# Kernel tuning notes

Hardware: AMD Instinct MI355X
Metric: run time of the kernel (lower is better)

The kernel has to match this reference:

```python
import jax, jax.numpy as jnp
import numpy as np

B, T, DIM, DZ = 512, 256, 128, 256
H = 2 * DZ  # LSTM hidden size (per direction)
RESIDUAL = False


def _lstm_cell(xt, h, c, Wih, Whh, bih, bhh):
    # PyTorch gate order: input, forget, cell, output
    g = xt @ Wih.T + bih + h @ Whh.T + bhh
    i, f, gg, o = jnp.split(g, 4, axis=-1)
    c2 = jax.nn.sigmoid(f) * c + jax.nn.sigmoid(i) * jnp.tanh(gg)
    h2 = jax.nn.sigmoid(o) * jnp.tanh(c2)
    return h2, c2


def _masked_lstm(xs, lengths, Wih, Whh, bih, bhh):
    # Packed-sequence semantics: state frozen and output zero past each length.
    Bn, Tn, _ = xs.shape
    Hn = Whh.shape[1]

    def step(carry, inp):
        h, c = carry
        xt, t = inp
        h2, c2 = _lstm_cell(xt, h, c, Wih, Whh, bih, bhh)
        m = (t < lengths)[:, None]
        h = jnp.where(m, h2, h)
        c = jnp.where(m, c2, c)
        return (h, c), jnp.where(m, h2, 0.0)

    init = (jnp.zeros((Bn, Hn), xs.dtype), jnp.zeros((Bn, Hn), xs.dtype))
    _, hs = jax.lax.scan(step, init, (xs.swapaxes(0, 1), jnp.arange(Tn)))
    return hs.swapaxes(0, 1)  # [B,T,H]


def setup_inputs() -> dict:
    key = jax.random.key(0)
    ks = jax.random.split(key, 24)
    rn = lambda k, *s: jax.random.normal(k, s, jnp.float32) * 0.02
    z = jnp.zeros
    return {
        "x": jax.random.normal(ks[0], (B, T, DIM), jnp.float32),
        "x_lengths": jax.random.randint(ks[1], (B,), 1, T + 1),
        "norm_g": jnp.ones((T, DIM)), "norm_b": z((T, DIM)),
        "We": rn(ks[2], DZ, DIM), "be": z((DZ,)),
        "Wih_f": rn(ks[3], 4 * H, DZ), "Whh_f": rn(ks[4], 4 * H, H),
        "bih_f": z((4 * H,)), "bhh_f": z((4 * H,)),
        "Wih_b": rn(ks[5], 4 * H, DZ), "Whh_b": rn(ks[6], 4 * H, H),
        "bih_b": z((4 * H,)), "bhh_b": z((4 * H,)),
        "W1e": rn(ks[7], H, 2 * H), "b1e": z((H,)),
        "W2e": rn(ks[8], DZ, H), "b2e": z((DZ,)),
        "Wd": rn(ks[9], DZ, DZ), "bd": z((DZ,)),
        "Wp1": rn(ks[10], DZ, DZ), "bp1": z((DZ,)),
        "Wp2": rn(ks[11], DIM, DZ), "bp2": z((DIM,)),
        "Wih_d": rn(ks[12], 4 * H, DZ + DIM), "Whh_d": rn(ks[13], 4 * H, H),
        "bih_d": z((4 * H,)), "bhh_d": z((4 * H,)),
        "W1d": rn(ks[14], DZ, H), "b1d": z((DZ,)),
        "W2d": rn(ks[15], DIM, DZ), "b2d": z((DIM,)),
    }


def _forward(x, x_lengths, norm_g, norm_b, We, be,
             Wih_f, Whh_f, bih_f, bhh_f, Wih_b, Whh_b, bih_b, bhh_b,
             W1e, b1e, W2e, b2e,
             Wd, bd, Wp1, bp1, Wp2, bp2,
             Wih_d, Whh_d, bih_d, bhh_d, W1d, b1d, W2d, b2d):
    # ----- encoder -----
    # LayerNorm over the last two dims [T, DIM] per sample
    mu = x.mean(axis=(1, 2), keepdims=True)
    var = x.var(axis=(1, 2), keepdims=True)
    xn = (x - mu) / jnp.sqrt(var + 1e-5) * norm_g + norm_b
    xe = jax.nn.relu(xn @ We.T + be)  # [B,T,DZ]

    hs_f = _masked_lstm(xe, x_lengths, Wih_f, Whh_f, bih_f, bhh_f)
    # backward direction: reverse each valid prefix, run, scatter back
    rev_idx = jnp.clip(x_lengths[:, None] - 1 - jnp.arange(T)[None, :], 0)  # [B,T]
    xe_rev = jnp.take_along_axis(xe, rev_idx[:, :, None], axis=1)
    hs_b_rev = _masked_lstm(xe_rev, x_lengths, Wih_b, Whh_b, bih_b, bhh_b)
    hs_b = jnp.take_along_axis(hs_b_rev, rev_idx[:, :, None], axis=1)
    valid = (jnp.arange(T)[None, :] < x_lengths[:, None])[:, :, None]
    out = jnp.concatenate([hs_f, jnp.where(valid, hs_b, 0.0)], axis=-1)  # [B,T,2H]
    out = out.sum(axis=1) / x_lengths[:, None].astype(x.dtype)
    out = jax.nn.relu(out @ W1e.T + b1e)
    zlat = out @ W2e.T + b2e  # [B,DZ]

    x0 = jax.nn.relu(zlat @ Wd.T + bd)
    pose0 = jax.nn.relu(x0 @ Wp1.T + bp1) @ Wp2.T + bp2  # [B,DIM]
    h0 = jnp.zeros((x.shape[0], H), x.dtype)

    def dstep(carry, _):
        h, c, pose = carry
        inp = jnp.concatenate([x0, pose], axis=1)
        h2, c2 = _lstm_cell(inp, h, c, Wih_d, Whh_d, bih_d, bhh_d)
        h_ = jax.nn.relu(h2 @ W1d.T + b1d)
        new_pose = h_ @ W2d.T + b2d
        if RESIDUAL:
            new_pose = new_pose + pose
        return (h2, c2, new_pose), new_pose

    _, poses = jax.lax.scan(dstep, (h0, h0, pose0), None, length=T)
    return poses.swapaxes(0, 1)  # [B,T,DIM]


def reference(x, x_lengths, norm_g, norm_b, We, be,
              Wih_f, Whh_f, bih_f, bhh_f, Wih_b, Whh_b, bih_b, bhh_b,
              W1e, b1e, W2e, b2e,
              Wd, bd, Wp1, bp1, Wp2, bp2,
              Wih_d, Whh_d, bih_d, bhh_d, W1d, b1d, W2d, b2d):
    dec = _forward(x, x_lengths, norm_g, norm_b, We, be,
                   Wih_f, Whh_f, bih_f, bhh_f, Wih_b, Whh_b, bih_b, bhh_b,
                   W1e, b1e, W2e, b2e,
                   Wd, bd, Wp1, bp1, Wp2, bp2,
                   Wih_d, Whh_d, bih_d, bhh_d, W1d, b1d, W2d, b2d)
    return (x, dec, x_lengths)
```

## Files before the change

### kernel.cpp

```cpp
#include <hip/hip_runtime.h>
#include <stdint.h>
#include <math.h>

typedef unsigned short u16;
typedef unsigned long long u64;
typedef short s16x8 __attribute__((ext_vector_type(8)));
typedef __bf16 bv8 __attribute__((ext_vector_type(8)));
typedef float f32x4 __attribute__((ext_vector_type(4)));

#define DEV static __device__ __forceinline__

DEV float b2f(u16 x){ union{unsigned u; float f;} v; v.u=((unsigned)x)<<16; return v.f; }
DEV u16 f2b(float f){ union{float f; unsigned u;} v; v.f=f; unsigned u=v.u; u += 0x7fff + ((u>>16)&1u); return (u16)(u>>16); }
DEV float sigm(float x){ return 1.f/(1.f+__expf(-x)); }
DEV float tanh_(float x){ float cx=fminf(fmaxf(x,-20.f),20.f); float e=__expf(2.f*cx); return (e-1.f)/(e+1.f); }
DEV f32x4 mfma16(bv8 a, bv8 b, f32x4 c){ return __builtin_amdgcn_mfma_f32_16x16x32_bf16(a,b,c,0,0,0); }
DEV bv8 ldf(const u16* p){ return __builtin_bit_cast(bv8, *(const s16x8*)p); }
DEV bv8 cvt(const s16x8& v){ return __builtin_bit_cast(bv8, v); }

DEV unsigned ald4(const unsigned* p){ return __hip_atomic_load(p, __ATOMIC_RELAXED, __HIP_MEMORY_SCOPE_AGENT); }

DEV void gld16(s16x8& d, const u16* p){
  asm volatile("global_load_dwordx4 %0, %1, off sc0 sc1" : "=&v"(d) : "v"(p));
}
DEV void gst8(u16* p, u64 v){
  asm volatile("global_store_dwordx2 %0, %1, off sc0 sc1" :: "v"(p), "v"(v) : "memory");
}
template<int N> DEV void wvm(){
  asm volatile("s_waitcnt vmcnt(%0)" :: "i"(N) : "memory");
  __builtin_amdgcn_sched_barrier(0);
}

DEV void arrive(unsigned* flags, int my, unsigned e){
  asm volatile("s_waitcnt vmcnt(0)" ::: "memory");
  __syncthreads();
  if (threadIdx.x==0)
    __hip_atomic_store(&flags[my*32], e, __ATOMIC_RELAXED, __HIP_MEMORY_SCOPE_AGENT);
}
DEV void waitflags(unsigned* flags, int lo, int n, unsigned e){
  int t = (int)threadIdx.x;
  if (t>=lo && t<lo+n){
    while (ald4(&flags[t*32]) < e) __builtin_amdgcn_s_sleep(1);
  }
  __syncthreads();
}

struct CvtJobs { const float* s[14]; u16* d[14]; int start[14]; };

__global__ __launch_bounds__(256) void cvt_w(CvtJobs J){
  int blk = blockIdx.x, tid = threadIdx.x;
  int j = 0;
  #pragma unroll
  for (int k=1;k<14;k++) if (blk >= J.start[k]) j = k;
  size_t idx = (size_t)(blk - J.start[j])*2048 + (size_t)tid*8;
  const f32x4* ps = (const f32x4*)(J.s[j] + idx);
  f32x4 a = ps[0], b = ps[1];
  s16x8 o;
  #pragma unroll
  for (int i=0;i<4;i++){ o[i]=(short)f2b(a[i]); o[4+i]=(short)f2b(b[i]); }
  *(s16x8*)(J.d[j] + idx) = o;
}

__global__ __launch_bounds__(256) void tr_w2d(const u16* __restrict__ in, u16* __restrict__ out){
  int idx = blockIdx.x*256 + threadIdx.x;
  int r = idx>>7, p = idx&127;
  out[idx] = in[p*256 + r];
}

__global__ __launch_bounds__(256) void pb_k(const float* __restrict__ Wihd, const float* __restrict__ b2d,
                                            float* __restrict__ pb){
  int g = blockIdx.x*256 + threadIdx.x;
  const float* row = Wihd + (size_t)g*384 + 256;
  float s = 0.f;
  for (int p=0;p<128;p++) s += row[p]*b2d[p];
  pb[g] = s;
}

__global__ __launch_bounds__(256) void ln_stats(const float* __restrict__ x,
                                                float* __restrict__ mu, float* __restrict__ rstd){
  int b = blockIdx.x;
  const float* xb = x + (size_t)b*32768;
  float s1=0.f, s2=0.f;
  for (int i = threadIdx.x*4; i < 32768; i += 256*4){
    f32x4 v = *(const f32x4*)(xb+i);
    #pragma unroll
    for (int j=0;j<4;j++){ float f = v[j]; s1+=f; s2+=f*f; }
  }
  #pragma unroll
  for (int o=32;o>0;o>>=1){ s1 += __shfl_down(s1,o); s2 += __shfl_down(s2,o); }
  __shared__ float r1[4], r2[4];
  int w = threadIdx.x>>6;
  if ((threadIdx.x&63)==0){ r1[w]=s1; r2[w]=s2; }
  __syncthreads();
  if (threadIdx.x==0){
    float a=0.f,c=0.f;
    for (int i=0;i<4;i++){ a+=r1[i]; c+=r2[i]; }
    float m=a/32768.f, v=c/32768.f-m*m;
    mu[b]=m; rstd[b]=1.f/sqrtf(v+1e-5f);
  }
}

__global__ __launch_bounds__(256) void ln_gemm(const float* __restrict__ x,
    const float* __restrict__ mu, const float* __restrict__ rstd,
    const float* __restrict__ g, const float* __restrict__ bn,
    const u16* __restrict__ Wb, const float* __restrict__ be, u16* __restrict__ xe){
  __shared__ __align__(16) u16 As[128*32];
  __shared__ __align__(16) u16 Ws[128*32];
  int tid=threadIdx.x, lane=tid&63, wid=tid>>6;
  int wr=wid>>1, wc=wid&1;
  long m0=(long)blockIdx.y*128, n0=(long)blockIdx.x*128;
  int lr=lane&15, lk=(lane>>4)*8;
  f32x4 acc[4][4];
  #pragma unroll
  for (int i=0;i<4;i++)
    #pragma unroll
    for (int j=0;j<4;j++) acc[i][j]=(f32x4){0.f,0.f,0.f,0.f};

  for (int k0=0;k0<128;k0+=32){
    __syncthreads();
    #pragma unroll
    for (int c=tid;c<512;c+=256){
      int row=c>>2, kb=(c&3)*8;
      long R=m0+row;
      int b=(int)(R>>8), tt=(int)(R&255);
      float m=mu[b], rs=rstd[b];
      const f32x4* px=(const f32x4*)(x + R*128 + k0+kb);
      const f32x4* pg=(const f32x4*)(g + tt*128 + k0+kb);
      const f32x4* pb=(const f32x4*)(bn + tt*128 + k0+kb);
      f32x4 x0=px[0], x1=px[1], g0=pg[0], g1=pg[1], b0=pb[0], b1=pb[1];
      s16x8 o;
      #pragma unroll
      for (int j=0;j<4;j++){
        o[j]   = (short)f2b((x0[j]-m)*rs*g0[j] + b0[j]);
        o[4+j] = (short)f2b((x1[j]-m)*rs*g1[j] + b1[j]);
      }
      *(s16x8*)(As + row*32 + kb) = o;
    }
    #pragma unroll
    for (int c=tid;c<512;c+=256){
      int row=c>>2, kb=(c&3)*8;
      *(s16x8*)(Ws + row*32 + kb) = *(const s16x8*)(Wb + (n0+row)*128 + k0+kb);
    }
    __syncthreads();
    bv8 af[4], bf[4];
    #pragma unroll
    for (int i=0;i<4;i++) af[i] = ldf(As + (wr*64+i*16+lr)*32 + lk);
    #pragma unroll
    for (int j=0;j<4;j++) bf[j] = ldf(Ws + (wc*64+j*16+lr)*32 + lk);
    #pragma unroll
    for (int i=0;i<4;i++)
      #pragma unroll
      for (int j=0;j<4;j++) acc[i][j] = mfma16(af[i], bf[j], acc[i][j]);
  }
  #pragma unroll
  for (int i=0;i<4;i++)
    #pragma unroll
    for (int j=0;j<4;j++)
      #pragma unroll
      for (int r=0;r<4;r++){
        int m = wr*64+i*16+(lane>>4)*4+r;
        int n = wc*64+j*16+lr;
        float v = acc[i][j][r] + be[n0+n];
        xe[(m0+m)*256 + n0+n] = f2b(fmaxf(v,0.f));
      }
}

template<int BM, int BN, bool RELU, bool OUTF32>
__global__ __launch_bounds__(256) void gemm_bt(const u16* __restrict__ A, int lda,
                                               const u16* __restrict__ W, int ldw,
                                               const float* __restrict__ bias1, const float* __restrict__ bias2,
                                               u16* __restrict__ Cb, float* __restrict__ Cf, int ldc, int K){
  constexpr int BK=32;
  constexpr int FM=BM/32, FN=BN/32;
  __shared__ __align__(16) u16 As[BM*BK];
  __shared__ __align__(16) u16 Ws[BN*BK];
  int tid=threadIdx.x, lane=tid&63, wid=tid>>6;
  int wr=wid>>1, wc=wid&1;
  long m0=(long)blockIdx.y*BM, n0=(long)blockIdx.x*BN;
  int lr=lane&15, lk=(lane>>4)*8;
  f32x4 acc[FM][FN];
  #pragma unroll
  for (int i=0;i<FM;i++)
    #pragma unroll
    for (int j=0;j<FN;j++) acc[i][j] = (f32x4){0.f,0.f,0.f,0.f};
  for (int k0=0;k0<K;k0+=BK){
    __syncthreads();
    #pragma unroll
    for (int c=tid;c<BM*4;c+=256){
      int row=c>>2, kb=(c&3)*8;
      *(s16x8*)(As + row*BK + kb) = *(const s16x8*)(A + (m0+row)*lda + k0+kb);
    }
    #pragma unroll
    for (int c=tid;c<BN*4;c+=256){
      int row=c>>2, kb=(c&3)*8;
      *(s16x8*)(Ws + row*BK + kb) = *(const s16x8*)(W + (n0+row)*ldw + k0+kb);
    }
    __syncthreads();
    bv8 af[FM], bf[FN];
    #pragma unroll
    for (int i=0;i<FM;i++) af[i] = ldf(As + (wr*(BM/2)+i*16+lr)*BK + lk);
    #pragma unroll
    for (int j=0;j<FN;j++) bf[j] = ldf(Ws + (wc*(BN/2)+j*16+lr)*BK + lk);
    #pragma unroll
    for (int i=0;i<FM;i++)
      #pragma unroll
      for (int j=0;j<FN;j++) acc[i][j] = mfma16(af[i], bf[j], acc[i][j]);
  }
  #pragma unroll
  for (int i=0;i<FM;i++)
    #pragma unroll
    for (int j=0;j<FN;j++)
      #pragma unroll
      for (int r=0;r<4;r++){
        int m = wr*(BM/2)+i*16+(lane>>4)*4+r;
        int n = wc*(BN/2)+j*16+lr;
        float v = acc[i][j][r];
        if (bias1) v += bias1[n0+n];
        if (bias2) v += bias2[n0+n];
        if (RELU) v = fmaxf(v,0.f);
        if (OUTF32) Cf[(m0+m)*ldc + n0+n] = v;
        else        Cb[(m0+m)*ldc + n0+n] = f2b(v);
      }
}

struct EncP {
  const u16* xe; const int* lens;
  const u16 *Wihf,*Whhf,*Wihb,*Whhb;
  const float *bif,*bhf,*bib,*bhb;
  u16 *hf0,*hf1,*hb0,*hb1,*pooled;
  unsigned* flags;
};

__global__ __launch_bounds__(256,1) void enc_persist(EncP P){
  __shared__ __align__(16) u16 Wl[64*776];
  __shared__ __align__(16) u16 Hs[128*16];
  const int tid=threadIdx.x, lane=tid&63, w=tid>>6;
  const int bx=blockIdx.x;
  const int grp=bx&7, kc=bx>>3;
  const int dir=grp>>2, bt=grp&3;
  const int lr=lane&15, lk=(lane>>4)*8;
  unsigned* flags = P.flags + grp*2048;
  const u16* Wih = dir? P.Wihb : P.Wihf;
  const u16* Whh = dir? P.Whhb : P.Whhf;
  const float* bi = dir? P.bib : P.bif;
  const float* bh = dir? P.bhb : P.bhf;
  u16* h0 = dir? P.hb0 : P.hf0;
  u16* h1 = dir? P.hb1 : P.hf1;

  for (int idx=tid; idx<64*96; idx+=256){
    int row=idx/96, col=(idx%96)*8;
    int g=row>>4, c=row&15;
    size_t grow=(size_t)(g*512 + kc*16 + c);
    const u16* src = (col<256)? (Wih + grow*256 + col) : (Whh + grow*512 + (col-256));
    *(s16x8*)(Wl + row*776 + col) = *(const s16x8*)src;
  }
  const int cg = kc*16 + lr;
  const float b_i=bi[cg]+bh[cg], b_f=bi[512+cg]+bh[512+cg];
  const float b_g=bi[1024+cg]+bh[1024+cg], b_o=bi[1536+cg]+bh[1536+cg];
  const int r0 = w*32 + lr, r1i = r0 + 16;
  const int slen0 = P.lens[bt*128+r0], slen1 = P.lens[bt*128+r1i];
  const u16* xb0 = P.xe + (size_t)(bt*128+r0)*65536;
  const u16* xb1 = P.xe + (size_t)(bt*128+r1i)*65536;
  int elen[2][4]; float cs[2][4], hh[2][4], asum[2][4];
  #pragma unroll
  for (int i=0;i<2;i++)
    #pragma unroll
    for (int r=0;r<4;r++){
      int m=w*32+i*16+(lane>>4)*4+r;
      elen[i][r]=P.lens[bt*128+m];
      cs[i][r]=0.f; hh[i][r]=0.f; asum[i][r]=0.f;
    }
  __syncthreads();

  auto xpart=[&](int t_, f32x4 (&xacc)[2][4]){
    int tt0 = dir? max(slen0-1-t_,0) : t_;
    int tt1 = dir? max(slen1-1-t_,0) : t_;
    const u16* xr0 = xb0 + (size_t)tt0*256;
    const u16* xr1 = xb1 + (size_t)tt1*256;
    #pragma unroll
    for (int k=0;k<4;k++)
      #pragma unroll
      for (int kk=0;kk<2;kk++){
        bv8 a0 = ldf(xr0 + k*64 + kk*32 + lk);
        bv8 a1 = ldf(xr1 + k*64 + kk*32 + lk);
        #pragma unroll
        for (int g=0;g<4;g++){
          bv8 bf = ldf(Wl + (g*16+lr)*776 + k*64 + kk*32 + lk);
          xacc[0][g]=mfma16(a0,bf,xacc[0][g]);
          xacc[1][g]=mfma16(a1,bf,xacc[1][g]);
        }
      }
  };

  f32x4 xacc[2][4];
  #pragma unroll
  for (int i=0;i<2;i++)
    #pragma unroll
    for (int g=0;g<4;g++) xacc[i][g]=(f32x4){0.f,0.f,0.f,0.f};
  xpart(0, xacc);

  for (int t=0;t<256;t++){
    const u16* hp = (t&1)? h1 : h0;
    u16*       hn = (t&1)? h0 : h1;
    waitflags(flags, 0, 32, (unsigned)t);
    f32x4 acc[2][4];
    #pragma unroll
    for (int i=0;i<2;i++)
      #pragma unroll
      for (int g=0;g<4;g++) acc[i][g]=xacc[i][g];
    {
      const u16* hr0 = hp + (size_t)(bt*128+r0)*512;
      const u16* hr1 = hp + (size_t)(bt*128+r1i)*512;
      s16x8 fb[2][8];
      auto issue=[&](int b, int k2){
        const u16* p0 = hr0 + k2*128;
        const u16* p1 = hr1 + k2*128;
        gld16(fb[b][0], p0+lk);    gld16(fb[b][1], p1+lk);
        gld16(fb[b][2], p0+32+lk); gld16(fb[b][3], p1+32+lk);
        gld16(fb[b][4], p0+64+lk); gld16(fb[b][5], p1+64+lk);
        gld16(fb[b][6], p0+96+lk); gld16(fb[b][7], p1+96+lk);
      };
      issue(0,0); issue(1,1);
      #pragma unroll
      for (int k2=0;k2<4;k2++){
        if (k2<3) wvm<8>(); else wvm<0>();
        const int b=k2&1;
        #pragma unroll
        for (int dk=0;dk<2;dk++)
          #pragma unroll
          for (int kk=0;kk<2;kk++){
            bv8 a0=cvt(fb[b][dk*4+kk*2]), a1=cvt(fb[b][dk*4+kk*2+1]);
            #pragma unroll
            for (int g=0;g<4;g++){
              bv8 bf=ldf(Wl + (g*16+lr)*776 + 256 + (2*k2+dk)*64 + kk*32 + lk);
              acc[0][g]=mfma16(a0,bf,acc[0][g]);
              acc[1][g]=mfma16(a1,bf,acc[1][g]);
            }
          }
        if (k2<2) issue(k2&1, k2+2);
      }
    }
    #pragma unroll
    for (int i=0;i<2;i++)
      #pragma unroll
      for (int r=0;r<4;r++){
        int m=w*32+i*16+(lane>>4)*4+r;
        if (t<elen[i][r]){
          float iv=sigm(acc[i][0][r]+b_i), fv=sigm(acc[i][1][r]+b_f);
          float gv=tanh_(acc[i][2][r]+b_g), ov=sigm(acc[i][3][r]+b_o);
          float c2=fv*cs[i][r]+iv*gv, h2v=ov*tanh_(c2);
          cs[i][r]=c2; hh[i][r]=h2v; asum[i][r]+=h2v;
        }
        Hs[m*16+lr]=f2b(hh[i][r]);
      }
    __syncthreads();
    #pragma unroll
    for (int q=0;q<2;q++){
      int cc=tid*2+q, sm=cc>>2, pt=cc&3;
      gst8(hn + (size_t)(bt*128+sm)*512 + kc*16 + pt*4, *(const u64*)(Hs + sm*16 + pt*4));
    }
    arrive(flags, kc, (unsigned)(t+1));
    #pragma unroll
    for (int i=0;i<2;i++)
      #pragma unroll
      for (int g=0;g<4;g++) xacc[i][g]=(f32x4){0.f,0.f,0.f,0.f};
    if (t<255) xpart(t+1, xacc);
  }
  #pragma unroll
  for (int i=0;i<2;i++)
    #pragma unroll
    for (int r=0;r<4;r++){
      int m=w*32+i*16+(lane>>4)*4+r;
      P.pooled[(size_t)(bt*128+m)*1024 + (size_t)dir*512 + cg]=f2b(asum[i][r]/(float)elen[i][r]);
    }
}

struct DecP {
  const u16 *Whhd, *Wcmp, *W1d, *W2d;
  const float *gix, *gp0, *pb, *b1d, *b2d;
  u16 *h0,*h1,*r1a,*r1b;
  float* outd;
  unsigned* flags;
};

__global__ __launch_bounds__(256,1) void dec_persist(DecP P){
  __shared__ __align__(16) u16 Wh [64*520];
  __shared__ __align__(16) u16 WcL[64*264];
  __shared__ __align__(16) u16 F12[16*520];
  __shared__ __align__(16) u16 Hs[64*16];
  const int tid=threadIdx.x, lane=tid&63, w=tid>>6;
  const int bx=blockIdx.x;
  const int grp=bx&7, kc=bx>>3;
  const int g0 = grp*64;
  const int lr=lane&15, lk=(lane>>4)*8;
  unsigned* flags = P.flags + grp*2048;

  for (int idx=tid; idx<64*64; idx+=256){
    int row=idx>>6, col=(idx&63)*8;
    int g=row>>4, c=row&15;
    size_t grow=(size_t)(g*512+kc*16+c);
    *(s16x8*)(Wh + row*520 + col) = *(const s16x8*)(P.Whhd + grow*512 + col);
  }
  for (int idx=tid; idx<64*32; idx+=256){
    int row=idx>>5, col=(idx&31)*8;
    int g=row>>4, c=row&15;
    size_t grow=(size_t)(g*512+kc*16+c);
    *(s16x8*)(WcL + row*264 + col) = *(const s16x8*)(P.Wcmp + grow*256 + col);
  }
  if (kc<16){
    for (int idx=tid; idx<16*64; idx+=256){
      int rr=idx>>6, col=(idx&63)*8;
      *(s16x8*)(F12 + rr*520 + col) = *(const s16x8*)(P.W1d + (size_t)(kc*16+rr)*512 + col);
    }
  } else if (kc<24){
    for (int idx=tid; idx<16*32; idx+=256){
      int rr=idx>>5, col=(idx&31)*8;
      *(s16x8*)(F12 + rr*264 + col) = *(const s16x8*)(P.W2d + (size_t)((kc-16)*16+rr)*256 + col);
    }
  }
  float gx[4][4]; float pbr[4];
  #pragma unroll
  for (int g=0;g<4;g++)
    #pragma unroll
    for (int r=0;r<4;r++){
      int m=w*16+(lane>>4)*4+r;
      gx[g][r]=P.gix[(size_t)(g0+m)*2048 + (size_t)g*512 + kc*16 + lr];
    }
  #pragma unroll
  for (int g=0;g<4;g++) pbr[g] = P.pb[(size_t)g*512 + kc*16 + lr];
  const float b1=(kc<16)? P.b1d[kc*16+lr] : 0.f;
  const float b2=(kc>=16&&kc<24)? P.b2d[(kc-16)*16+lr] : 0.f;
  const int ar = w*16 + lr;
  float cs[4];
  f32x4 gh[4];
  #pragma unroll
  for (int r=0;r<4;r++) cs[r]=0.f;
  #pragma unroll
  for (int g=0;g<4;g++) gh[g]=(f32x4){0.f,0.f,0.f,0.f};
  __syncthreads();

  for (int t=0;t<256;t++){
    const u16* r1rd = (t&1)? P.r1b : P.r1a;
    u16* hn = (t&1)? P.h0 : P.h1;
    f32x4 acc[4];
    if (t==0){
      #pragma unroll
      for (int g=0;g<4;g++)
        #pragma unroll
        for (int r=0;r<4;r++){
          int m=w*16+(lane>>4)*4+r;
          acc[g][r] = gx[g][r] + P.gp0[(size_t)(g0+m)*2048 + (size_t)g*512 + kc*16 + lr];
        }
    } else {
      waitflags(flags, 32, 16, (unsigned)t);
      #pragma unroll
      for (int g=0;g<4;g++){
        acc[g] = (f32x4){gx[g][0]+pbr[g], gx[g][1]+pbr[g], gx[g][2]+pbr[g], gx[g][3]+pbr[g]};
        acc[g] = acc[g] + gh[g];
      }
      const u16* rb = r1rd + (size_t)(g0+ar)*256;
      s16x8 fb[8];
      #pragma unroll
      for (int k=0;k<4;k++){
        gld16(fb[k*2],   rb + k*64 + lk);
        gld16(fb[k*2+1], rb + k*64 + 32 + lk);
      }
      wvm<0>();
      #pragma unroll
      for (int k=0;k<4;k++)
        #pragma unroll
        for (int kk=0;kk<2;kk++){
          bv8 a=cvt(fb[k*2+kk]);
          #pragma unroll
          for (int g=0;g<4;g++){
            bv8 bf=ldf(WcL + (g*16+lr)*264 + k*64 + kk*32 + lk);
            acc[g]=mfma16(a,bf,acc[g]);
          }
        }
    }
    #pragma unroll
    for (int r=0;r<4;r++){
      float iv=sigm(acc[0][r]), fv=sigm(acc[1][r]);
      float gv=tanh_(acc[2][r]), ov=sigm(acc[3][r]);
      float c2=fv*cs[r]+iv*gv, h2v=ov*tanh_(c2);
      cs[r]=c2;
      int m=w*16+(lane>>4)*4+r;
      Hs[m*16+lr]=f2b(h2v);
    }
    __syncthreads();
    {
      int sm=tid>>2, pt=tid&3;
      gst8(hn + (size_t)(g0+sm)*512 + kc*16 + pt*4, *(const u64*)(Hs + sm*16 + pt*4));
    }
    arrive(flags, kc, (unsigned)(t+1));
    if (kc>=16 && kc<24 && t>0){
      const u16* rb = r1rd + (size_t)(g0+ar)*256;
      f32x4 fa2=(f32x4){0.f,0.f,0.f,0.f};
      s16x8 fb[8];
      #pragma unroll
      for (int k=0;k<4;k++){
        gld16(fb[k*2],   rb + k*64 + lk);
        gld16(fb[k*2+1], rb + k*64 + 32 + lk);
      }
      wvm<0>();
      #pragma unroll
      for (int k=0;k<4;k++)
        #pragma unroll
        for (int kk=0;kk<2;kk++){
          bv8 a=cvt(fb[k*2+kk]);
          bv8 bf=ldf(F12 + lr*264 + k*64 + kk*32 + lk);
          fa2=mfma16(a,bf,fa2);
        }
      int pc=(kc-16)*16+lr;
      #pragma unroll
      for (int r=0;r<4;r++){
        int m=w*16+(lane>>4)*4+r;
        __builtin_nontemporal_store(fa2[r]+b2, P.outd + (size_t)(g0+m)*32768 + (size_t)(t-1)*128 + pc);
      }
    }
    waitflags(flags, 0, 32, (unsigned)(t+1));
    f32x4 gn[4]; f32x4 fa=(f32x4){0.f,0.f,0.f,0.f};
    #pragma unroll
    for (int g=0;g<4;g++) gn[g]=(f32x4){0.f,0.f,0.f,0.f};
    {
      const u16* hb = hn + (size_t)(g0+ar)*512;
      s16x8 fb[2][8];
      auto issue=[&](int b, int h4){
        const u16* p = hb + h4*256;
        #pragma unroll
        for (int k=0;k<4;k++){
          gld16(fb[b][k*2],   p + k*64 + lk);
          gld16(fb[b][k*2+1], p + k*64 + 32 + lk);
        }
      };
      issue(0,0); issue(1,1);
      #pragma unroll
      for (int h4=0;h4<2;h4++){
        if (h4==0) wvm<8>(); else wvm<0>();
        #pragma unroll
        for (int k=0;k<4;k++)
          #pragma unroll
          for (int kk=0;kk<2;kk++){
            bv8 a=cvt(fb[h4][k*2+kk]);
            int col = h4*256 + k*64 + kk*32;
            #pragma unroll
            for (int g=0;g<4;g++){
              bv8 bf=ldf(Wh + (g*16+lr)*520 + col + lk);
              gn[g]=mfma16(a,bf,gn[g]);
            }
            if (kc<16){
              bv8 bf=ldf(F12 + lr*520 + col + lk);
              fa=mfma16(a,bf,fa);
            }
          }
      }
    }
    #pragma unroll
    for (int g=0;g<4;g++) gh[g]=gn[g];
    if (kc<16){
      u16* r1w = (t&1)? P.r1a : P.r1b;
      #pragma unroll
      for (int r=0;r<4;r++){
        int m=w*16+(lane>>4)*4+r;
        Hs[m*16+lr]=f2b(fmaxf(fa[r]+b1,0.f));
      }
      __syncthreads();
      {
        int sm=tid>>2, pt=tid&3;
        gst8(r1w + (size_t)(g0+sm)*256 + kc*16 + pt*4, *(const u64*)(Hs + sm*16 + pt*4));
      }
      arrive(flags, 32+kc, (unsigned)(t+1));
    }
  }
  if (kc>=16 && kc<24){
    waitflags(flags, 32, 16, 256u);
    const u16* rb = P.r1a + (size_t)(g0+ar)*256;
    f32x4 fa2=(f32x4){0.f,0.f,0.f,0.f};
    s16x8 fb[8];
    #pragma unroll
    for (int k=0;k<4;k++){
      gld16(fb[k*2],   rb + k*64 + lk);
      gld16(fb[k*2+1], rb + k*64 + 32 + lk);
    }
    wvm<0>();
    #pragma unroll
    for (int k=0;k<4;k++)
      #pragma unroll
      for (int kk=0;kk<2;kk++){
        bv8 a=cvt(fb[k*2+kk]);
        bv8 bf=ldf(F12 + lr*264 + k*64 + kk*32 + lk);
        fa2=mfma16(a,bf,fa2);
      }
    int pc=(kc-16)*16+lr;
    #pragma unroll
    for (int r=0;r<4;r++){
      int m=w*16+(lane>>4)*4+r;
      __builtin_nontemporal_store(fa2[r]+b2, P.outd + (size_t)(g0+m)*32768 + (size_t)255*128 + pc);
    }
  }
}

__global__ __launch_bounds__(512) void len_cast(const int* __restrict__ lens, float* __restrict__ out){
  int i = threadIdx.x;
  if (i < 512) out[i] = (float)lens[i];
}

extern "C" void kernel_launch(void* const* d_in, const int* in_sizes, int n_in,
                              void* d_out, int out_size, void* d_ws, size_t ws_size,
                              hipStream_t stream){
  (void)in_sizes; (void)n_in; (void)out_size; (void)ws_size;
  const float* x      = (const float*)d_in[0];
  const int*   lens   = (const int*)d_in[1];
  const float* ng     = (const float*)d_in[2];
  const float* nb     = (const float*)d_in[3];
  const float* We     = (const float*)d_in[4];
  const float* be     = (const float*)d_in[5];
  const float* Wih_f  = (const float*)d_in[6];
  const float* Whh_f  = (const float*)d_in[7];
  const float* bih_f  = (const float*)d_in[8];
  const float* bhh_f  = (const float*)d_in[9];
  const float* Wih_b  = (const float*)d_in[10];
  const float* Whh_b  = (const float*)d_in[11];
  const float* bih_b  = (const float*)d_in[12];
  const float* bhh_b  = (const float*)d_in[13];
  const float* W1e    = (const float*)d_in[14];
  const float* b1e    = (const float*)d_in[15];
  const float* W2e    = (const float*)d_in[16];
  const float* b2e    = (const float*)d_in[17];
  const float* Wd     = (const float*)d_in[18];
  const float* bd     = (const float*)d_in[19];
  const float* Wp1    = (const float*)d_in[20];
  const float* bp1    = (const float*)d_in[21];
  const float* Wp2    = (const float*)d_in[22];
  const float* bp2    = (const float*)d_in[23];
  const float* Wih_d  = (const float*)d_in[24];
  const float* Whh_d  = (const float*)d_in[25];
  const float* bih_d  = (const float*)d_in[26];
  const float* bhh_d  = (const float*)d_in[27];
  const float* W1d    = (const float*)d_in[28];
  const float* b1d    = (const float*)d_in[29];
  const float* W2d    = (const float*)d_in[30];
  const float* b2d    = (const float*)d_in[31];

  char* p = (char*)d_ws;
  auto carve = [&](size_t bytes)->void*{ void* r=(void*)p; p += (bytes+255)&~(size_t)255; return r; };
  float* mu   = (float*)carve(512*4);
  float* rstd = (float*)carve(512*4);
  u16* xe     = (u16*)carve((size_t)33554432*2);
  u16* wWe  = (u16*)carve(32768*2);
  u16* wIhf = (u16*)carve(524288*2);
  u16* wHhf = (u16*)carve(1048576*2);
  u16* wIhb = (u16*)carve(524288*2);
  u16* wHhb = (u16*)carve(1048576*2);
  u16* wW1e = (u16*)carve(524288*2);
  u16* wW2e = (u16*)carve(131072*2);
  u16* wWd  = (u16*)carve(65536*2);
  u16* wWp1 = (u16*)carve(65536*2);
  u16* wWp2 = (u16*)carve(32768*2);
  u16* wIhd = (u16*)carve(786432*2);
  u16* wHhd = (u16*)carve(1048576*2);
  u16* wW1d = (u16*)carve(131072*2);
  u16* wW2d = (u16*)carve(32768*2);
  u16* wW2dT  = (u16*)carve(32768*2);
  u16* wWcomp = (u16*)carve(524288*2);
  float* pbv  = (float*)carve(2048*4);
  float* gp0f = (float*)carve((size_t)1048576*4);
  u16* hf0  = (u16*)carve(524288);
  u16* hf1  = (u16*)carve(524288);
  u16* hb0  = (u16*)carve(524288);
  u16* hb1  = (u16*)carve(524288);
  u16* hd0  = (u16*)carve(524288);
  u16* hd1  = (u16*)carve(524288);
  u16* r1a  = (u16*)carve(262144);
  u16* r1b  = (u16*)carve(262144);
  u16* pooled = (u16*)carve(1048576);
  u16* out1   = (u16*)carve(524288);
  u16* zlat   = (u16*)carve(262144);
  u16* x0     = (u16*)carve(262144);
  u16* t0     = (u16*)carve(262144);
  float* gix  = (float*)carve(4194304);
  u16* pose   = (u16*)carve(131072);
  unsigned* barflags = (unsigned*)carve(16*2048*4);

  float* out_x   = (float*)d_out;
  float* out_dec = out_x + 16777216;
  float* out_len = out_x + 33554432;

  hipMemcpyAsync(out_x, x, (size_t)16777216*4, hipMemcpyDeviceToDevice, stream);
  hipMemsetAsync(hf0,0,524288,stream);
  hipMemsetAsync(hb0,0,524288,stream);
  hipMemsetAsync(barflags,0,16*2048*4,stream);

  CvtJobs J;
  const float* srcs[14] = {We,Wih_f,Whh_f,Wih_b,Whh_b,W1e,W2e,Wd,Wp1,Wp2,Wih_d,Whh_d,W1d,W2d};
  u16* dsts[14] = {wWe,wIhf,wHhf,wIhb,wHhb,wW1e,wW2e,wWd,wWp1,wWp2,wIhd,wHhd,wW1d,wW2d};
  int ns[14] = {32768,524288,1048576,524288,1048576,524288,131072,65536,65536,32768,786432,1048576,131072,32768};
  int blk=0;
  for (int i=0;i<14;i++){ J.s[i]=srcs[i]; J.d[i]=dsts[i]; J.start[i]=blk; blk += ns[i]/2048; }
  cvt_w<<<blk,256,0,stream>>>(J);

  tr_w2d<<<128,256,0,stream>>>(wW2d, wW2dT);
  pb_k<<<8,256,0,stream>>>(Wih_d, b2d, pbv);
  gemm_bt<64,64,false,false><<<dim3(4,32),256,0,stream>>>(wIhd+256,384, wW2dT,128, nullptr,nullptr, wWcomp,nullptr,256,128);

  ln_stats<<<512,256,0,stream>>>(x,mu,rstd);
  ln_gemm<<<dim3(2,1024),256,0,stream>>>(x,mu,rstd,ng,nb,wWe,be,xe);

  EncP EP = {xe,lens,wIhf,wHhf,wIhb,wHhb,bih_f,bhh_f,bih_b,bhh_b,hf0,hf1,hb0,hb1,pooled,barflags};
  {
    void* ea[] = {&EP};
    if (hipLaunchCooperativeKernel((void*)enc_persist, dim3(256), dim3(256), ea, 0, stream) != hipSuccess)
      enc_persist<<<256,256,0,stream>>>(EP);
  }

  gemm_bt<64,64,true ,false><<<dim3(8,8),256,0,stream>>>(pooled,1024,wW1e,1024,b1e,nullptr,out1,nullptr,512,1024);
  gemm_bt<64,64,false,false><<<dim3(4,8),256,0,stream>>>(out1,512,wW2e,512,b2e,nullptr,zlat,nullptr,256,512);
  gemm_bt<64,64,true ,false><<<dim3(4,8),256,0,stream>>>(zlat,256,wWd,256,bd,nullptr,x0,nullptr,256,256);
  gemm_bt<64,64,true ,false><<<dim3(4,8),256,0,stream>>>(x0,256,wWp1,256,bp1,nullptr,t0,nullptr,256,256);
  gemm_bt<64,64,false,false><<<dim3(2,8),256,0,stream>>>(t0,256,wWp2,256,bp2,nullptr,pose,nullptr,128,256);
  gemm_bt<64,128,false,true><<<dim3(16,8),256,0,stream>>>(x0,256,wIhd,384,bih_d,bhh_d,nullptr,gix,2048,256);
  gemm_bt<64,128,false,true><<<dim3(16,8),256,0,stream>>>(pose,128,wIhd+256,384,nullptr,nullptr,nullptr,gp0f,2048,128);

  DecP DP = {wHhd,wWcomp,wW1d,wW2d, gix,gp0f,pbv,b1d,b2d, hd0,hd1,r1a,r1b, out_dec, barflags + 8*2048};
  {
    void* da[] = {&DP};
    if (hipLaunchCooperativeKernel((void*)dec_persist, dim3(256), dim3(256), da, 0, stream) != hipSuccess)
      dec_persist<<<256,256,0,stream>>>(DP);
  }

  len_cast<<<1,512,0,stream>>>(lens,out_len);
}
```

Before: 4.379 ms.

## Double encoder persistent block to 512 threads with one row tile per wave

The encoder persistent kernel now runs 8 waves per block instead of 4, so each wave handles a single 16-row tile rather than two. The input-projection x rows are prefetched as raw registers during the previous step, and all 16 h loads are issued at once with a two-phase wait. The flag polling now uses an inline cache-bypassing load instead of an atomic load. The goal is more in-flight memory parallelism and shorter per-wave MFMA chains on the serial recurrence, at the cost of more registers per thread and possible occupancy limits at 512 threads.

Result: faster. 4.117 ms (-6.0%).

```diff
diff --git a/kernel.cpp b/kernel.cpp
--- a/kernel.cpp
+++ b/kernel.cpp
@@ -23,6 +23,9 @@
 DEV void gld16(s16x8& d, const u16* p){
   asm volatile("global_load_dwordx4 %0, %1, off sc0 sc1" : "=&v"(d) : "v"(p));
 }
+DEV void gldc16(s16x8& d, const u16* p){
+  asm volatile("global_load_dwordx4 %0, %1, off" : "=&v"(d) : "v"(p));
+}
 DEV void gst8(u16* p, u64 v){
   asm volatile("global_store_dwordx2 %0, %1, off sc0 sc1" :: "v"(p), "v"(v) : "memory");
 }
@@ -40,7 +43,12 @@
 DEV void waitflags(unsigned* flags, int lo, int n, unsigned e){
   int t = (int)threadIdx.x;
   if (t>=lo && t<lo+n){
-    while (ald4(&flags[t*32]) < e) __builtin_amdgcn_s_sleep(1);
+    unsigned v;
+    do {
+      asm volatile("global_load_dword %0, %1, off sc0 sc1\ns_waitcnt vmcnt(0)" : "=&v"(v) : "v"(flags + t*32) : "memory");
+      if (v>=e) break;
+      __builtin_amdgcn_s_sleep(1);
+    } while (1);
   }
   __syncthreads();
 }
@@ -231,7 +239,7 @@
   unsigned* flags;
 };
 
-__global__ __launch_bounds__(256,1) void enc_persist(EncP P){
+__global__ __launch_bounds__(512,1) void enc_persist(EncP P){
   __shared__ __align__(16) u16 Wl[64*776];
   __shared__ __align__(16) u16 Hs[128*16];
   const int tid=threadIdx.x, lane=tid&63, w=tid>>6;
@@ -247,7 +255,7 @@
   u16* h0 = dir? P.hb0 : P.hf0;
   u16* h1 = dir? P.hb1 : P.hf1;
 
-  for (int idx=tid; idx<64*96; idx+=256){
+  for (int idx=tid; idx<64*96; idx+=512){
     int row=idx/96, col=(idx%96)*8;
     int g=row>>4, c=row&15;
     size_t grow=(size_t)(g*512 + kc*16 + c);
@@ -257,122 +265,93 @@
   const int cg = kc*16 + lr;
   const float b_i=bi[cg]+bh[cg], b_f=bi[512+cg]+bh[512+cg];
   const float b_g=bi[1024+cg]+bh[1024+cg], b_o=bi[1536+cg]+bh[1536+cg];
-  const int r0 = w*32 + lr, r1i = r0 + 16;
-  const int slen0 = P.lens[bt*128+r0], slen1 = P.lens[bt*128+r1i];
+  const int r0 = w*16 + lr;
+  const int slen0 = P.lens[bt*128+r0];
   const u16* xb0 = P.xe + (size_t)(bt*128+r0)*65536;
-  const u16* xb1 = P.xe + (size_t)(bt*128+r1i)*65536;
-  int elen[2][4]; float cs[2][4], hh[2][4], asum[2][4];
-  #pragma unroll
-  for (int i=0;i<2;i++)
-    #pragma unroll
-    for (int r=0;r<4;r++){
-      int m=w*32+i*16+(lane>>4)*4+r;
-      elen[i][r]=P.lens[bt*128+m];
-      cs[i][r]=0.f; hh[i][r]=0.f; asum[i][r]=0.f;
-    }
+  int elen[4]; float cs[4], hh[4], asum[4];
+  #pragma unroll
+  for (int r=0;r<4;r++){
+    int m=w*16+(lane>>4)*4+r;
+    elen[r]=P.lens[bt*128+m];
+    cs[r]=0.f; hh[r]=0.f; asum[r]=0.f;
+  }
   __syncthreads();
 
-  auto xpart=[&](int t_, f32x4 (&xacc)[2][4]){
-    int tt0 = dir? max(slen0-1-t_,0) : t_;
-    int tt1 = dir? max(slen1-1-t_,0) : t_;
-    const u16* xr0 = xb0 + (size_t)tt0*256;
-    const u16* xr1 = xb1 + (size_t)tt1*256;
-    #pragma unroll
-    for (int k=0;k<4;k++)
-      #pragma unroll
-      for (int kk=0;kk<2;kk++){
-        bv8 a0 = ldf(xr0 + k*64 + kk*32 + lk);
-        bv8 a1 = ldf(xr1 + k*64 + kk*32 + lk);
-        #pragma unroll
-        for (int g=0;g<4;g++){
-          bv8 bf = ldf(Wl + (g*16+lr)*776 + k*64 + kk*32 + lk);
-          xacc[0][g]=mfma16(a0,bf,xacc[0][g]);
-          xacc[1][g]=mfma16(a1,bf,xacc[1][g]);
-        }
-      }
+  s16x8 rx[8];
+  auto issue_rx=[&](int t_){
+    int tt = dir? max(slen0-1-t_,0) : t_;
+    const u16* xr = xb0 + (size_t)tt*256;
+    #pragma unroll
+    for (int j=0;j<8;j++) gldc16(rx[j], xr + j*32 + lk);
   };
-
-  f32x4 xacc[2][4];
-  #pragma unroll
-  for (int i=0;i<2;i++)
-    #pragma unroll
-    for (int g=0;g<4;g++) xacc[i][g]=(f32x4){0.f,0.f,0.f,0.f};
-  xpart(0, xacc);
+  issue_rx(0);
 
   for (int t=0;t<256;t++){
     const u16* hp = (t&1)? h1 : h0;
     u16*       hn = (t&1)? h0 : h1;
     waitflags(flags, 0, 32, (unsigned)t);
-    f32x4 acc[2][4];
-    #pragma unroll
-    for (int i=0;i<2;i++)
-      #pragma unroll
-      for (int g=0;g<4;g++) acc[i][g]=xacc[i][g];
+    s16x8 fb[16];
     {
-      const u16* hr0 = hp + (size_t)(bt*128+r0)*512;
-      const u16* hr1 = hp + (size_t)(bt*128+r1i)*512;
-      s16x8 fb[2][8];
-      auto issue=[&](int b, int k2){
-        const u16* p0 = hr0 + k2*128;
-        const u16* p1 = hr1 + k2*128;
-        gld16(fb[b][0], p0+lk);    gld16(fb[b][1], p1+lk);
-        gld16(fb[b][2], p0+32+lk); gld16(fb[b][3], p1+32+lk);
-        gld16(fb[b][4], p0+64+lk); gld16(fb[b][5], p1+64+lk);
-        gld16(fb[b][6], p0+96+lk); gld16(fb[b][7], p1+96+lk);
-      };
-      issue(0,0); issue(1,1);
-      #pragma unroll
-      for (int k2=0;k2<4;k2++){
-        if (k2<3) wvm<8>(); else wvm<0>();
-        const int b=k2&1;
-        #pragma unroll
-        for (int dk=0;dk<2;dk++)
-          #pragma unroll
-          for (int kk=0;kk<2;kk++){
-            bv8 a0=cvt(fb[b][dk*4+kk*2]), a1=cvt(fb[b][dk*4+kk*2+1]);
-            #pragma unroll
-            for (int g=0;g<4;g++){
-              bv8 bf=ldf(Wl + (g*16+lr)*776 + 256 + (2*k2+dk)*64 + kk*32 + lk);
-              acc[0][g]=mfma16(a0,bf,acc[0][g]);
-              acc[1][g]=mfma16(a1,bf,acc[1][g]);
-            }
-          }
-        if (k2<2) issue(k2&1, k2+2);
-      }
-    }
-    #pragma unroll
-    for (int i=0;i<2;i++)
-      #pragma unroll
-      for (int r=0;r<4;r++){
-        int m=w*32+i*16+(lane>>4)*4+r;
-        if (t<elen[i][r]){
-          float iv=sigm(acc[i][0][r]+b_i), fv=sigm(acc[i][1][r]+b_f);
-          float gv=tanh_(acc[i][2][r]+b_g), ov=sigm(acc[i][3][r]+b_o);
-          float c2=fv*cs[i][r]+iv*gv, h2v=ov*tanh_(c2);
-          cs[i][r]=c2; hh[i][r]=h2v; asum[i][r]+=h2v;
-        }
-        Hs[m*16+lr]=f2b(hh[i][r]);
-      }
+      const u16* hr = hp + (size_t)(bt*128+r0)*512;
+      #pragma unroll
+      for (int j=0;j<16;j++) gld16(fb[j], hr + j*32 + lk);
+    }
+    f32x4 acc[4];
+    #pragma unroll
+    for (int g=0;g<4;g++) acc[g]=(f32x4){0.f,0.f,0.f,0.f};
+    #pragma unroll
+    for (int j=0;j<8;j++){
+      bv8 a = cvt(rx[j]);
+      #pragma unroll
+      for (int g=0;g<4;g++){
+        bv8 bf = ldf(Wl + (g*16+lr)*776 + j*32 + lk);
+        acc[g]=mfma16(a,bf,acc[g]);
+      }
+    }
+    wvm<8>();
+    #pragma unroll
+    for (int j=0;j<8;j++){
+      bv8 a = cvt(fb[j]);
+      #pragma unroll
+      for (int g=0;g<4;g++){
+        bv8 bf = ldf(Wl + (g*16+lr)*776 + 256 + j*32 + lk);
+        acc[g]=mfma16(a,bf,acc[g]);
+      }
+    }
+    wvm<0>();
+    #pragma unroll
+    for (int j=8;j<16;j++){
+      bv8 a = cvt(fb[j]);
+      #pragma unroll
+      for (int g=0;g<4;g++){
+        bv8 bf = ldf(Wl + (g*16+lr)*776 + 256 + j*32 + lk);
+        acc[g]=mfma16(a,bf,acc[g]);
+      }
+    }
+    #pragma unroll
+    for (int r=0;r<4;r++){
+      int m=w*16+(lane>>4)*4+r;
+      if (t<elen[r]){
+        float iv=sigm(acc[0][r]+b_i), fv=sigm(acc[1][r]+b_f);
+        float gv=tanh_(acc[2][r]+b_g), ov=sigm(acc[3][r]+b_o);
+        float c2=fv*cs[r]+iv*gv, h2v=ov*tanh_(c2);
+        cs[r]=c2; hh[r]=h2v; asum[r]+=h2v;
+      }
+      Hs[m*16+lr]=f2b(hh[r]);
+    }
     __syncthreads();
-    #pragma unroll
-    for (int q=0;q<2;q++){
-      int cc=tid*2+q, sm=cc>>2, pt=cc&3;
+    {
+      int sm=tid>>2, pt=tid&3;
       gst8(hn + (size_t)(bt*128+sm)*512 + kc*16 + pt*4, *(const u64*)(Hs + sm*16 + pt*4));
     }
     arrive(flags, kc, (unsigned)(t+1));
-    #pragma unroll
-    for (int i=0;i<2;i++)
-      #pragma unroll
-      for (int g=0;g<4;g++) xacc[i][g]=(f32x4){0.f,0.f,0.f,0.f};
-    if (t<255) xpart(t+1, xacc);
-  }
-  #pragma unroll
-  for (int i=0;i<2;i++)
-    #pragma unroll
-    for (int r=0;r<4;r++){
-      int m=w*32+i*16+(lane>>4)*4+r;
-      P.pooled[(size_t)(bt*128+m)*1024 + (size_t)dir*512 + cg]=f2b(asum[i][r]/(float)elen[i][r]);
-    }
+    if (t<255) issue_rx(t+1);
+  }
+  #pragma unroll
+  for (int r=0;r<4;r++){
+    int m=w*16+(lane>>4)*4+r;
+    P.pooled[(size_t)(bt*128+m)*1024 + (size_t)dir*512 + cg]=f2b(asum[r]/(float)elen[r]);
+  }
 }
 
 struct DecP {
@@ -709,8 +688,8 @@
   EncP EP = {xe,lens,wIhf,wHhf,wIhb,wHhb,bih_f,bhh_f,bih_b,bhh_b,hf0,hf1,hb0,hb1,pooled,barflags};
   {
     void* ea[] = {&EP};
-    if (hipLaunchCooperativeKernel((void*)enc_persist, dim3(256), dim3(256), ea, 0, stream) != hipSuccess)
-      enc_persist<<<256,256,0,stream>>>(EP);
+    if (hipLaunchCooperativeKernel((void*)enc_persist, dim3(256), dim3(512), ea, 0, stream) != hipSuccess)
+      enc_persist<<<256,512,0,stream>>>(EP);
   }
 
   gemm_bt<64,64,true ,false><<<dim3(8,8),256,0,stream>>>(pooled,1024,wW1e,1024,b1e,nullptr,out1,nullptr,512,1024);
```
